# Performance work log

Measured on AMD Instinct MI355X. Metric: run time of the kernel, lower is better.

## Reference

```python
import jax, jax.numpy as jnp
import numpy as np

# init config (matches init_kwargs)
NO_TRANS = False
SPATIAL_SCALE = 0.0625
POOLED = 7
SAMPLES = 2          # sampling_ratio (sample_per_part)
TRANS_STD = 0.1

B, C, H, W = 2, 256, 96, 96
N_ROIS = 512


def setup_inputs() -> dict:
    key = jax.random.key(0)
    k1, k2, k3, k4, k5 = jax.random.split(key, 5)
    bottom_data = jax.random.normal(k1, (B, C, H, W), dtype=jnp.float32)
    img = H / SPATIAL_SCALE  # image-space extent (1536)
    bidx = jax.random.randint(k2, (N_ROIS,), 0, B).astype(jnp.float32)
    xy1 = jax.random.uniform(k3, (N_ROIS, 2), minval=0.0, maxval=0.7 * img)
    wh = jax.random.uniform(k4, (N_ROIS, 2), minval=0.05 * img, maxval=0.3 * img)
    bottom_rois = jnp.concatenate([bidx[:, None], xy1, xy1 + wh], axis=1)  # [N,5]
    bottom_trans = jax.random.normal(k5, (N_ROIS, 2, POOLED, POOLED), dtype=jnp.float32)
    return {"bottom_data": bottom_data, "bottom_rois": bottom_rois, "bottom_trans": bottom_trans}


def _deform_psroi_pool(feat, rois, trans):
    # feat [B,C,H,W], rois [N,5], trans [N,2,P,P] -> out [N,C,P,P]
    Hf, Wf = feat.shape[2], feat.shape[3]
    b = rois[:, 0].astype(jnp.int32)                                    # [N]
    # CUDA kernel rounds roi coords, shifts by -0.5
    x1 = jnp.round(rois[:, 1]) * SPATIAL_SCALE - 0.5
    y1 = jnp.round(rois[:, 2]) * SPATIAL_SCALE - 0.5
    x2 = (jnp.round(rois[:, 3]) + 1.0) * SPATIAL_SCALE - 0.5
    y2 = (jnp.round(rois[:, 4]) + 1.0) * SPATIAL_SCALE - 0.5
    rw = jnp.maximum(x2 - x1, 0.1)
    rh = jnp.maximum(y2 - y1, 0.1)
    bin_w = rw / POOLED
    bin_h = rh / POOLED
    sub_w = bin_w / SAMPLES
    sub_h = bin_h / SAMPLES

    grid = jnp.arange(POOLED, dtype=feat.dtype)
    # part_size == pooled_size and group_size == 1 -> part_h=ph, part_w=pw, class 0
    if NO_TRANS:
        trans_x = jnp.zeros((rois.shape[0], POOLED, POOLED), feat.dtype)
        trans_y = trans_x
    else:
        trans_x = trans[:, 0] * TRANS_STD  # [N,P,P]
        trans_y = trans[:, 1] * TRANS_STD

    # bin start coords per (n, ph, pw)
    wstart = grid[None, None, :] * bin_w[:, None, None] + x1[:, None, None] + trans_x * rw[:, None, None]
    hstart = grid[None, :, None] * bin_h[:, None, None] + y1[:, None, None] + trans_y * rh[:, None, None]

    s = jnp.arange(SAMPLES, dtype=feat.dtype)
    # sample coords [N,P,P,S(ih),S(iw)]
    w = wstart[:, :, :, None, None] + s[None, None, None, None, :] * sub_w[:, None, None, None, None]
    h = hstart[:, :, :, None, None] + s[None, None, None, :, None] * sub_h[:, None, None, None, None]

    valid = (w >= -0.5) & (w <= Wf - 0.5) & (h >= -0.5) & (h <= Hf - 0.5)
    wc = jnp.clip(w, 0.0, Wf - 1.0)
    hc = jnp.clip(h, 0.0, Hf - 1.0)
    x0 = jnp.floor(wc); y0 = jnp.floor(hc)
    dx = wc - x0; dy = hc - y0
    x0i = x0.astype(jnp.int32); y0i = y0.astype(jnp.int32)
    x1i = jnp.ceil(wc).astype(jnp.int32); y1i = jnp.ceil(hc).astype(jnp.int32)

    feat_hwc = jnp.transpose(feat, (0, 2, 3, 1))  # [B,H,W,C]
    bb = b[:, None, None, None, None]

    def gather(yi, xi):
        return feat_hwc[bb, yi, xi]  # [N,P,P,S,S,C]

    w00 = ((1.0 - dx) * (1.0 - dy))[..., None]
    w01 = (dx * (1.0 - dy))[..., None]
    w10 = ((1.0 - dx) * dy)[..., None]
    w11 = (dx * dy)[..., None]
    val = (w00 * gather(y0i, x0i) + w01 * gather(y0i, x1i)
           + w10 * gather(y1i, x0i) + w11 * gather(y1i, x1i))
    val = jnp.where(valid[..., None], val, 0.0)

    ssum = val.sum(axis=(3, 4))                              # [N,P,P,C]
    count = valid.astype(feat.dtype).sum(axis=(3, 4))        # [N,P,P]
    out = jnp.where(count[..., None] > 0, ssum / jnp.maximum(count[..., None], 1.0), 0.0)
    return jnp.transpose(out, (0, 3, 1, 2))                  # [N,C,P,P]


def reference(bottom_data, bottom_rois, bottom_trans):
    return _deform_psroi_pool(bottom_data, bottom_rois, bottom_trans)
```

## Files before the change

### kernel.cpp

```cpp
#include <hip/hip_runtime.h>

#define B_      2
#define C_      256
#define H_      96
#define W_      96
#define HW_     (H_ * W_)
#define P_      7
#define PP_     (P_ * P_)
#define NROIS_  512
#define SCALE_  0.0625f
#define TSTD_   0.1f

#define NGROUP_ 8
#define GC_     (C_ / NGROUP_)

typedef float vf4 __attribute__((ext_vector_type(4)));

__device__ __forceinline__ unsigned f2bf(float f) {
    union { float f; unsigned u; } x; x.f = f;
    return (x.u + 0x7fffu + ((x.u >> 16) & 1u)) >> 16;
}
__device__ __forceinline__ float bf_lo(unsigned u) {
    union { unsigned i; float f; } x; x.i = u << 16; return x.f;
}
__device__ __forceinline__ float bf_hi(unsigned u) {
    union { unsigned i; float f; } x; x.i = u & 0xffff0000u; return x.f;
}

__global__ __launch_bounds__(256) void nchw_to_gp_bf16(const float* __restrict__ in,
                                                       ushort* __restrict__ out) {
    __shared__ float tile[32][36];
    const int b   = blockIdx.z;
    const int g   = blockIdx.x & (NGROUP_ - 1);
    const int p0  = (blockIdx.x >> 3) * 32;
    const int c0  = g * 32;
    const int tid = threadIdx.x;

    const float* src = in + (size_t)b * (C_ * HW_);
    ushort*      dst = out + ((size_t)(b * NGROUP_ + g) * HW_) * GC_;

    {
        const int cr = tid >> 3;
        const int pq = (tid & 7) * 4;
        const vf4 v = __builtin_nontemporal_load(
            (const vf4*)&src[(size_t)(c0 + cr) * HW_ + p0 + pq]);
        *(vf4*)&tile[cr][pq] = v;
    }
    __syncthreads();

    {
        const int p  = tid >> 3;
        const int cq = (tid & 7) * 4;
        uint2 o;
        o.x = f2bf(tile[cq + 0][p]) | (f2bf(tile[cq + 1][p]) << 16);
        o.y = f2bf(tile[cq + 2][p]) | (f2bf(tile[cq + 3][p]) << 16);
        *(uint2*)&((unsigned*)dst)[(size_t)(p0 + p) * (GC_ / 2) + (cq >> 1)] = o;
    }
}

__global__ __launch_bounds__(256, 4) void dpsroi_pool7(const ushort* __restrict__ feat,
                                                       const float* __restrict__ rois,
                                                       const float* __restrict__ trans,
                                                       float* __restrict__ out) {
    __shared__ float sout[GC_ * PP_];

    const int blk = blockIdx.x;
    const int g   = blk & (NGROUP_ - 1);
    const int n   = blk >> 3;
    const int tid = threadIdx.x;
    const int bin = tid >> 2;
    const int ch0 = (tid & 3) * 8;

    const int   broi = (int)rois[n * 5 + 0];
    const float x1 = rintf(rois[n * 5 + 1]) * SCALE_ - 0.5f;
    const float y1 = rintf(rois[n * 5 + 2]) * SCALE_ - 0.5f;
    const float x2 = (rintf(rois[n * 5 + 3]) + 1.0f) * SCALE_ - 0.5f;
    const float y2 = (rintf(rois[n * 5 + 4]) + 1.0f) * SCALE_ - 0.5f;
    const float rw = fmaxf(x2 - x1, 0.1f);
    const float rh = fmaxf(y2 - y1, 0.1f);
    const float bin_w = rw * (1.0f / 7.0f);
    const float bin_h = rh * (1.0f / 7.0f);
    const float sub_w = bin_w * 0.5f;
    const float sub_h = bin_h * 0.5f;

    const ushort* fb = feat + ((size_t)(broi * NGROUP_ + g) * HW_) * GC_ + ch0;

    if (bin < PP_) {
        const int pi = bin / P_;
        const int pj = bin - pi * P_;
        const float tx = trans[((n * 2 + 0) * P_ + pi) * P_ + pj] * TSTD_;
        const float ty = trans[((n * 2 + 1) * P_ + pi) * P_ + pj] * TSTD_;
        const float wstart = (float)pj * bin_w + x1 + tx * rw;
        const float hstart = (float)pi * bin_h + y1 + ty * rh;

        float wt[16];
        int   ofs[16];
        int   cnt = 0;
#pragma unroll
        for (int s = 0; s < 4; ++s) {
            const float w = wstart + (float)(s & 1) * sub_w;
            const float h = hstart + (float)(s >> 1) * sub_h;
            const bool valid = (w >= -0.5f) & (w <= (float)W_ - 0.5f) &
                               (h >= -0.5f) & (h <= (float)H_ - 0.5f);
            cnt += valid ? 1 : 0;
            const float vf = valid ? 1.0f : 0.0f;
            const float wc  = fminf(fmaxf(w, 0.0f), (float)(W_ - 1));
            const float hc  = fminf(fmaxf(h, 0.0f), (float)(H_ - 1));
            const float x0f = floorf(wc), y0f = floorf(hc);
            const float dx  = wc - x0f,   dy  = hc - y0f;
            const int   x0  = (int)x0f,   y0  = (int)y0f;
            const int   xp  = (int)ceilf(wc), yp = (int)ceilf(hc);
            wt[4 * s + 0] = vf * (1.0f - dx) * (1.0f - dy);
            wt[4 * s + 1] = vf * dx * (1.0f - dy);
            wt[4 * s + 2] = vf * (1.0f - dx) * dy;
            wt[4 * s + 3] = vf * dx * dy;
            ofs[4 * s + 0] = y0 * W_ + x0;
            ofs[4 * s + 1] = y0 * W_ + xp;
            ofs[4 * s + 2] = yp * W_ + x0;
            ofs[4 * s + 3] = yp * W_ + xp;
        }

        uint4 v[16];
#pragma unroll
        for (int i = 0; i < 16; ++i)
            v[i] = *(const uint4*)(fb + (size_t)ofs[i] * GC_);

        float acc[8] = {0.f, 0.f, 0.f, 0.f, 0.f, 0.f, 0.f, 0.f};
#pragma unroll
        for (int i = 0; i < 16; ++i) {
            const float wgt = wt[i];
            acc[0] += wgt * bf_lo(v[i].x);
            acc[1] += wgt * bf_hi(v[i].x);
            acc[2] += wgt * bf_lo(v[i].y);
            acc[3] += wgt * bf_hi(v[i].y);
            acc[4] += wgt * bf_lo(v[i].z);
            acc[5] += wgt * bf_hi(v[i].z);
            acc[6] += wgt * bf_lo(v[i].w);
            acc[7] += wgt * bf_hi(v[i].w);
        }

        const float inv = (cnt > 0) ? (1.0f / (float)cnt) : 0.0f;
#pragma unroll
        for (int j = 0; j < 8; ++j)
            sout[(ch0 + j) * PP_ + bin] = acc[j] * inv;
    }

    __syncthreads();
    float* outn = out + ((size_t)n * C_ + g * GC_) * PP_;
    for (int f = tid; f < GC_ * PP_; f += 256)
        __builtin_nontemporal_store(sout[f], &outn[f]);
}

extern "C" void kernel_launch(void* const* d_in, const int* in_sizes, int n_in,
                              void* d_out, int out_size, void* d_ws, size_t ws_size,
                              hipStream_t stream) {
    const float* feat  = (const float*)d_in[0];
    const float* rois  = (const float*)d_in[1];
    const float* trans = (const float*)d_in[2];
    float* out = (float*)d_out;

    ushort* gp = (ushort*)d_ws;
    dim3 tb(256);
    dim3 tg((HW_ / 32) * NGROUP_, 1, B_);
    nchw_to_gp_bf16<<<tg, tb, 0, stream>>>(feat, gp);
    dpsroi_pool7<<<NROIS_ * NGROUP_, 256, 0, stream>>>(gp, rois, trans, out);
}
```

Measured before the change: 90.29 us.

## Factor bilinear sampling into separable hat weights over a deduplicated pixel window

Rewrites the 2x2 sub-sample bilinear gather as a separable tent-weight sum over a small pixel window anchored at the first sample's floor. Each feature pixel is loaded once, so the 16 gathers become 9 fixed loads plus conditional extra rows and columns when the bin spans more pixels. This cuts duplicate gather traffic and FMAs when sub-samples share pixels. The cost is data-dependent branches and extra weight math. The window assumes sub-sample spacing stays under about two pixels, which holds for these ROI sizes.

```diff
diff --git a/kernel.cpp b/kernel.cpp
--- a/kernel.cpp
+++ b/kernel.cpp
@@ -26,6 +26,7 @@
 __device__ __forceinline__ float bf_hi(unsigned u) {
     union { unsigned i; float f; } x; x.i = u & 0xffff0000u; return x.f;
 }
+__device__ __forceinline__ float hat(float d) { return fmaxf(0.0f, 1.0f - fabsf(d)); }
 
 __global__ __launch_bounds__(256) void nchw_to_gp_bf16(const float* __restrict__ in,
                                                        ushort* __restrict__ out) {
@@ -47,7 +48,6 @@
         *(vf4*)&tile[cr][pq] = v;
     }
     __syncthreads();
-
     {
         const int p  = tid >> 3;
         const int cq = (tid & 7) * 4;
@@ -58,7 +58,7 @@
     }
 }
 
-__global__ __launch_bounds__(256, 4) void dpsroi_pool7(const ushort* __restrict__ feat,
+__global__ __launch_bounds__(256, 4) void dpsroi_pool8(const ushort* __restrict__ feat,
                                                        const float* __restrict__ rois,
                                                        const float* __restrict__ trans,
                                                        float* __restrict__ out) {
@@ -90,54 +90,88 @@
         const int pj = bin - pi * P_;
         const float tx = trans[((n * 2 + 0) * P_ + pi) * P_ + pj] * TSTD_;
         const float ty = trans[((n * 2 + 1) * P_ + pi) * P_ + pj] * TSTD_;
-        const float wstart = (float)pj * bin_w + x1 + tx * rw;
-        const float hstart = (float)pi * bin_h + y1 + ty * rh;
-
-        float wt[16];
-        int   ofs[16];
-        int   cnt = 0;
-#pragma unroll
-        for (int s = 0; s < 4; ++s) {
-            const float w = wstart + (float)(s & 1) * sub_w;
-            const float h = hstart + (float)(s >> 1) * sub_h;
-            const bool valid = (w >= -0.5f) & (w <= (float)W_ - 0.5f) &
-                               (h >= -0.5f) & (h <= (float)H_ - 0.5f);
-            cnt += valid ? 1 : 0;
-            const float vf = valid ? 1.0f : 0.0f;
-            const float wc  = fminf(fmaxf(w, 0.0f), (float)(W_ - 1));
-            const float hc  = fminf(fmaxf(h, 0.0f), (float)(H_ - 1));
-            const float x0f = floorf(wc), y0f = floorf(hc);
-            const float dx  = wc - x0f,   dy  = hc - y0f;
-            const int   x0  = (int)x0f,   y0  = (int)y0f;
-            const int   xp  = (int)ceilf(wc), yp = (int)ceilf(hc);
-            wt[4 * s + 0] = vf * (1.0f - dx) * (1.0f - dy);
-            wt[4 * s + 1] = vf * dx * (1.0f - dy);
-            wt[4 * s + 2] = vf * (1.0f - dx) * dy;
-            wt[4 * s + 3] = vf * dx * dy;
-            ofs[4 * s + 0] = y0 * W_ + x0;
-            ofs[4 * s + 1] = y0 * W_ + xp;
-            ofs[4 * s + 2] = yp * W_ + x0;
-            ofs[4 * s + 3] = yp * W_ + xp;
-        }
-
-        uint4 v[16];
-#pragma unroll
-        for (int i = 0; i < 16; ++i)
-            v[i] = *(const uint4*)(fb + (size_t)ofs[i] * GC_);
-
+        const float w0 = (float)pj * bin_w + x1 + tx * rw;
+        const float h0 = (float)pi * bin_h + y1 + ty * rh;
+        const float w1 = w0 + sub_w;
+        const float h1 = h0 + sub_h;
+
+        const int vw0 = (w0 >= -0.5f) & (w0 <= (float)W_ - 0.5f);
+        const int vw1 = (w1 >= -0.5f) & (w1 <= (float)W_ - 0.5f);
+        const int vh0 = (h0 >= -0.5f) & (h0 <= (float)H_ - 0.5f);
+        const int vh1 = (h1 >= -0.5f) & (h1 <= (float)H_ - 0.5f);
+        const int cnt = (vw0 + vw1) * (vh0 + vh1);
+
+        const float wc0 = fminf(fmaxf(w0, 0.0f), (float)(W_ - 1));
+        const float wc1 = fminf(fmaxf(w1, 0.0f), (float)(W_ - 1));
+        const float hc0 = fminf(fmaxf(h0, 0.0f), (float)(H_ - 1));
+        const float hc1 = fminf(fmaxf(h1, 0.0f), (float)(H_ - 1));
+
+        const int x_lo = (int)floorf(wc0);
+        const int y_lo = (int)floorf(hc0);
+        const float fvw0 = (float)vw0, fvw1 = (float)vw1;
+        const float fvh0 = (float)vh0, fvh1 = (float)vh1;
+
+        float WX[5], WY[5];
+#pragma unroll
+        for (int k = 0; k < 5; ++k) {
+            const float xx = (float)(x_lo + k);
+            const float yy = (float)(y_lo + k);
+            WX[k] = fvw0 * hat(wc0 - xx) + fvw1 * hat(wc1 - xx);
+            WY[k] = fvh0 * hat(hc0 - yy) + fvh1 * hat(hc1 - yy);
+        }
+
+        const int base = y_lo * W_ + x_lo;
         float acc[8] = {0.f, 0.f, 0.f, 0.f, 0.f, 0.f, 0.f, 0.f};
-#pragma unroll
-        for (int i = 0; i < 16; ++i) {
-            const float wgt = wt[i];
-            acc[0] += wgt * bf_lo(v[i].x);
-            acc[1] += wgt * bf_hi(v[i].x);
-            acc[2] += wgt * bf_lo(v[i].y);
-            acc[3] += wgt * bf_hi(v[i].y);
-            acc[4] += wgt * bf_lo(v[i].z);
-            acc[5] += wgt * bf_hi(v[i].z);
-            acc[6] += wgt * bf_lo(v[i].w);
-            acc[7] += wgt * bf_hi(v[i].w);
-        }
+
+#define ACCUM(J, K, V)                                                         \
+        {                                                                      \
+            const float wgt = WY[J] * WX[K];                                   \
+            acc[0] += wgt * bf_lo((V).x);  acc[1] += wgt * bf_hi((V).x);       \
+            acc[2] += wgt * bf_lo((V).y);  acc[3] += wgt * bf_hi((V).y);       \
+            acc[4] += wgt * bf_lo((V).z);  acc[5] += wgt * bf_hi((V).z);       \
+            acc[6] += wgt * bf_lo((V).w);  acc[7] += wgt * bf_hi((V).w);       \
+        }
+#define LOADPX(J, K) (*(const uint4*)(fb + (size_t)(base + (J) * W_ + (K)) * GC_))
+
+        {
+            uint4 v[9];
+#pragma unroll
+            for (int j = 0; j < 3; ++j)
+#pragma unroll
+                for (int k = 0; k < 3; ++k)
+                    v[j * 3 + k] = LOADPX(j, k);
+#pragma unroll
+            for (int j = 0; j < 3; ++j)
+#pragma unroll
+                for (int k = 0; k < 3; ++k)
+                    ACCUM(j, k, v[j * 3 + k]);
+        }
+#pragma unroll
+        for (int k = 3; k < 5; ++k) {
+            if (WX[k] > 0.0f) {
+                uint4 v[3];
+#pragma unroll
+                for (int j = 0; j < 3; ++j) v[j] = LOADPX(j, k);
+#pragma unroll
+                for (int j = 0; j < 3; ++j) ACCUM(j, k, v[j]);
+#pragma unroll
+                for (int j = 3; j < 5; ++j) {
+                    if (WY[j] > 0.0f) { const uint4 c = LOADPX(j, k); ACCUM(j, k, c); }
+                }
+            }
+        }
+#pragma unroll
+        for (int j = 3; j < 5; ++j) {
+            if (WY[j] > 0.0f) {
+                uint4 v[3];
+#pragma unroll
+                for (int k = 0; k < 3; ++k) v[k] = LOADPX(j, k);
+#pragma unroll
+                for (int k = 0; k < 3; ++k) ACCUM(j, k, v[k]);
+            }
+        }
+#undef ACCUM
+#undef LOADPX
 
         const float inv = (cnt > 0) ? (1.0f / (float)cnt) : 0.0f;
 #pragma unroll
@@ -163,5 +197,5 @@
     dim3 tb(256);
     dim3 tg((HW_ / 32) * NGROUP_, 1, B_);
     nchw_to_gp_bf16<<<tg, tb, 0, stream>>>(feat, gp);
-    dpsroi_pool7<<<NROIS_ * NGROUP_, 256, 0, stream>>>(gp, rois, trans, out);
-}
+    dpsroi_pool8<<<NROIS_ * NGROUP_, 256, 0, stream>>>(gp, rois, trans, out);
+}
```

Measured after the change: 91.70 us. No clear change (+1.6%).
